# Kernel optimization log

Measured on AMD Instinct MI355X. Metric: run time of the kernel, lower is better.

## Reference

```python
import jax, jax.numpy as jnp
import numpy as np

WINDOW = 512      # sliding window size (causal: keys in [m-WINDOW+1, m])
NEG_INF = -1e30   # large negative instead of -inf for fp16/bf16 safety


def setup_inputs() -> dict:
    key = jax.random.key(0)
    kq, kk, kv = jax.random.split(key, 3)
    B, S, H, Hk, D = 1, 8192, 32, 8, 128
    q = jax.random.normal(kq, (B, S, H, D), dtype=jnp.float32)
    k = jax.random.normal(kk, (B, S, Hk, D), dtype=jnp.float32)
    v = jax.random.normal(kv, (B, S, Hk, D), dtype=jnp.float32)
    return {"q": q, "k": k, "v": v}


def _swa_causal(q, k, v, window):
    """Causal sliding-window attention with GQA, banded (no SxS matrix)."""
    B, S, H, D = q.shape
    Hk = k.shape[2]
    G = H // Hk                      # query heads per kv head
    C = window                        # query block size
    nb = S // C                       # number of query blocks (S divisible by C here)
    L = 2 * window - 1                # kv window width per query block
    pad = window - 1
    scale = 1.0 / jnp.sqrt(jnp.asarray(D, q.dtype))

    # pad keys/values at the front so every block can gather a full window
    kp = jnp.pad(k, ((0, 0), (pad, 0), (0, 0), (0, 0)))
    vp = jnp.pad(v, ((0, 0), (pad, 0), (0, 0), (0, 0)))

    # block queries: [B, nb, C, Hk, G, D]
    qb = q.reshape(B, nb, C, Hk, G, D)

    # kv windows: block n sees padded positions [n*C, n*C + L)
    starts = jnp.arange(nb) * C                      # [nb]
    idx = starts[:, None] + jnp.arange(L)[None, :]   # [nb, L] padded coords
    kw = kp[:, idx]                                  # [B, nb, L, Hk, D]
    vw = vp[:, idx]                                  # [B, nb, L, Hk, D]

    # banded scores: [B, nb, Hk, G, C, L]
    scores = jnp.einsum('bnchgd,bnlhd->bnhgcl', qb, kw) * scale

    # mask: query i (global m = n*C + i), kv slot j (global n_pos = n*C + j - pad)
    # causal window: i <= j <= i + window - 1 ; plus n_pos >= 0
    i = jnp.arange(C)
    j = jnp.arange(L)
    band = (j[None, :] >= i[:, None]) & (j[None, :] <= i[:, None] + window - 1)  # [C, L]
    valid_n = (starts[:, None] + j[None, :] - pad) >= 0                          # [nb, L]
    mask = band[None, :, :] & valid_n[:, None, :]                                # [nb, C, L]

    scores = jnp.where(mask[:, None, None, :, :][None], scores, NEG_INF)
    p = jax.nn.softmax(scores, axis=-1)              # [B, nb, Hk, G, C, L]

    o = jnp.einsum('bnhgcl,bnlhd->bnchgd', p, vw)    # [B, nb, C, Hk, G, D]
    return o.reshape(B, S, H, D)


def reference(q, k, v):
    return _swa_causal(q, k, v, WINDOW)
```

## Files before the change

kernel.cpp:

```cpp
#include <hip/hip_runtime.h>

#define NH   32
#define NHK  8
#define D    128
#define QB   64
#define KB   64
#define NT   128

typedef float f32x4 __attribute__((ext_vector_type(4)));
typedef short bf16x8 __attribute__((ext_vector_type(8)));
typedef unsigned int uint4v __attribute__((ext_vector_type(4)));

__device__ __forceinline__ unsigned cvtpk(float lo, float hi) {
  unsigned r;
  asm("v_cvt_pk_bf16_f32 %0, %1, %2" : "=v"(r) : "v"(lo), "v"(hi));
  return r;
}
__device__ __forceinline__ void gload16(const void* g, void* l) {
  __builtin_amdgcn_global_load_lds(
      (__attribute__((address_space(1))) void*)g,
      (__attribute__((address_space(3))) void*)l, 16, 0, 0);
}

__device__ __forceinline__ int kidx(int j, int col) {
  return (((j >> 1) << 8) + ((j & 1) << 7) + col) ^ (((j >> 1) & 15) << 3);
}
__device__ __forceinline__ int vidx(int d, int j) {
  return (((d >> 1) << 7) + ((d & 1) << 6) + j) ^ (((d >> 1) & 15) << 3);
}

__global__ __launch_bounds__(256)
void prep_kv(const float* __restrict__ kg, const float* __restrict__ vg,
             short* __restrict__ kpre, short* __restrict__ vpre)
{
  int blk = blockIdx.x;
  int tid = threadIdx.x;
  bool isV = blk >= (NHK * NT);
  int lb   = isV ? blk - NHK * NT : blk;
  int hk   = lb >> 7;
  int t    = lb & 127;
  if (!isV) {
    int j  = tid >> 2;
    int dq = (tid & 3) * 32;
    const float* kp = kg + ((size_t)(t*KB + j) * NHK + hk) * D + dq;
    short* dst = kpre + (((size_t)(hk*NT + t)) << 13);
    #pragma unroll
    for (int c = 0; c < 4; ++c) {
      float4 a  = *(const float4*)(kp + c*8);
      float4 b2 = *(const float4*)(kp + c*8 + 4);
      uint4v u;
      u[0] = cvtpk(a.x, a.y);   u[1] = cvtpk(a.z, a.w);
      u[2] = cvtpk(b2.x, b2.y); u[3] = cvtpk(b2.z, b2.w);
      *(uint4v*)&dst[kidx(j, dq + c*8)] = u;
    }
  } else {
    int d0 = (tid & 31) * 4;
    int j0 = (tid >> 5) * 8;
    float tv[8][4];
    #pragma unroll
    for (int r = 0; r < 8; ++r) {
      float4 x = *(const float4*)(vg + ((size_t)(t*KB + j0 + r) * NHK + hk) * D + d0);
      tv[r][0]=x.x; tv[r][1]=x.y; tv[r][2]=x.z; tv[r][3]=x.w;
    }
    short* dst = vpre + (((size_t)(hk*NT + t)) << 13);
    #pragma unroll
    for (int c = 0; c < 4; ++c) {
      int d = d0 + c;
      uint4v u;
      u[0] = cvtpk(tv[0][c], tv[1][c]);
      u[1] = cvtpk(tv[2][c], tv[3][c]);
      u[2] = cvtpk(tv[4][c], tv[5][c]);
      u[3] = cvtpk(tv[6][c], tv[7][c]);
      *(uint4v*)&dst[vidx(d, j0)] = u;
    }
  }
}

__global__ __launch_bounds__(256, 3)
void swa_fwd(const float* __restrict__ qg, const short* __restrict__ kpre,
             const short* __restrict__ vpre, float* __restrict__ og)
{
  __shared__ __align__(16) short lds_k[KB * D];
  __shared__ __align__(16) short lds_v[KB * D];

  const int tid  = threadIdx.x;
  const int lane = tid & 63;
  const int w    = tid >> 6;
  const int il16 = lane & 15;
  const int g    = lane >> 4;

  int b    = blockIdx.x;
  int lidx = (b & 7) * 512 + (b >> 3);
  int hk   = lidx >> 9;
  int rem  = lidx & 511;
  int bq   = rem >> 2;
  int h    = hk * 4 + (rem & 3);
  int qs   = bq * QB;

  const float qscale = 0.088388347648318447f * 1.4426950408889634f;

  bf16x8 qf[4];
  {
    const float* qp = qg + ((size_t)(qs + 16*w + il16) * NH + h) * D + 8*g;
    #pragma unroll
    for (int ks = 0; ks < 4; ++ks) {
      float4 a = *(const float4*)(qp + 32*ks);
      float4 c = *(const float4*)(qp + 32*ks + 4);
      uint4v u;
      u[0] = cvtpk(a.x*qscale, a.y*qscale);
      u[1] = cvtpk(a.z*qscale, a.w*qscale);
      u[2] = cvtpk(c.x*qscale, c.y*qscale);
      u[3] = cvtpk(c.z*qscale, c.w*qscale);
      qf[ks] = __builtin_bit_cast(bf16x8, u);
    }
  }

  f32x4 acc_o[8];
  #pragma unroll
  for (int dt = 0; dt < 8; ++dt)
    #pragma unroll
    for (int r = 0; r < 4; ++r) acc_o[dt][r] = 0.0f;

  float l0 = 0.0f, l1 = 0.0f, l2 = 0.0f, l3 = 0.0f;

  const int iw_min = qs + 16*w;
  int t_lo = qs >= 512 ? (qs - 512) >> 6 : 0;
  int t_hi = qs >> 6;

  const short* gkb = kpre + (((size_t)hk * NT) << 13);
  const short* gvb = vpre + (((size_t)hk * NT) << 13);
  const int lo = w * 2048;
  const int go = lo + lane * 8;

  for (int t = t_lo; t <= t_hi; ++t) {
    const int kt = t * KB;

    {
      const short* gk = gkb + ((size_t)t << 13);
      const short* gv = gvb + ((size_t)t << 13);
      #pragma unroll
      for (int i = 0; i < 4; ++i) gload16(gk + go + i*512, &lds_k[0] + lo + i*512);
      #pragma unroll
      for (int i = 0; i < 4; ++i) gload16(gv + go + i*512, &lds_v[0] + lo + i*512);
    }
    asm volatile("s_waitcnt vmcnt(0)" ::: "memory");
    __builtin_amdgcn_s_barrier();
    __builtin_amdgcn_sched_barrier(0);

    bool skip = (kt > iw_min + 15) || (kt + KB - 1 < iw_min - 511);
    if (!skip) {
      f32x4 acc_s[4];
      #pragma unroll
      for (int jt = 0; jt < 4; ++jt)
        #pragma unroll
        for (int r = 0; r < 4; ++r) acc_s[jt][r] = 0.0f;

      __builtin_amdgcn_s_setprio(1);
      #pragma unroll
      for (int ks = 0; ks < 4; ++ks) {
        #pragma unroll
        for (int jt = 0; jt < 4; ++jt) {
          bf16x8 a = *(const bf16x8*)&lds_k[kidx(16*jt + il16, 32*ks + 8*g)];
          acc_s[jt] = __builtin_amdgcn_mfma_f32_16x16x32_bf16(a, qf[ks], acc_s[jt], 0, 0, 0);
        }
      }
      __builtin_amdgcn_s_setprio(0);

      bool do_causal = (kt + KB - 1 > iw_min);
      bool do_window = (kt < iw_min + 15 - 511);
      if (do_causal || do_window) {
        int base0 = kt - iw_min + 4*g - il16;
        #pragma unroll
        for (int jt = 0; jt < 4; ++jt)
          #pragma unroll
          for (int r = 0; r < 4; ++r) {
            int delta = base0 + 16*jt + r;
            if ((do_causal && delta > 0) || (do_window && delta < -511))
              acc_s[jt][r] = -1e30f;
          }
      }

      float p[4][4];
      #pragma unroll
      for (int jt = 0; jt < 4; ++jt)
        #pragma unroll
        for (int r = 0; r < 4; ++r)
          p[jt][r] = __builtin_amdgcn_exp2f(acc_s[jt][r]);
      l0 += p[0][0] + p[1][0] + p[2][0] + p[3][0];
      l1 += p[0][1] + p[1][1] + p[2][1] + p[3][1];
      l2 += p[0][2] + p[1][2] + p[2][2] + p[3][2];
      l3 += p[0][3] + p[1][3] + p[2][3] + p[3][3];

      #pragma unroll
      for (int kstep = 0; kstep < 2; ++kstep) {
        unsigned A0 = cvtpk(p[2*kstep+0][0], p[2*kstep+0][1]);
        unsigned B0 = cvtpk(p[2*kstep+0][2], p[2*kstep+0][3]);
        unsigned C0 = cvtpk(p[2*kstep+1][0], p[2*kstep+1][1]);
        unsigned D0 = cvtpk(p[2*kstep+1][2], p[2*kstep+1][3]);
        asm("v_permlane32_swap_b32 %0, %1" : "+v"(A0), "+v"(C0));
        asm("v_permlane32_swap_b32 %0, %1" : "+v"(B0), "+v"(D0));
        asm("v_permlane16_swap_b32 %0, %1" : "+v"(A0), "+v"(C0));
        asm("v_permlane16_swap_b32 %0, %1" : "+v"(B0), "+v"(D0));
        uint4v pu; pu[0] = A0; pu[1] = B0; pu[2] = C0; pu[3] = D0;
        bf16x8 pb = __builtin_bit_cast(bf16x8, pu);

        __builtin_amdgcn_s_setprio(1);
        #pragma unroll
        for (int dt = 0; dt < 8; ++dt) {
          bf16x8 a = *(const bf16x8*)&lds_v[vidx(16*dt + il16, 32*kstep + 8*g)];
          acc_o[dt] = __builtin_amdgcn_mfma_f32_16x16x32_bf16(a, pb, acc_o[dt], 0, 0, 0);
        }
        __builtin_amdgcn_s_setprio(0);
      }
    }
    if (t < t_hi) __builtin_amdgcn_s_barrier();
  }

  float l_lane = (l0 + l1) + (l2 + l3);
  l_lane += __shfl_xor(l_lane, 16);
  l_lane += __shfl_xor(l_lane, 32);
  float inv_l = 1.0f / l_lane;

  const size_t orow = ((size_t)(qs + 16*w + il16) * NH + h) * D;
  #pragma unroll
  for (int dt = 0; dt < 8; ++dt) {
    float4 o;
    o.x = acc_o[dt][0] * inv_l;
    o.y = acc_o[dt][1] * inv_l;
    o.z = acc_o[dt][2] * inv_l;
    o.w = acc_o[dt][3] * inv_l;
    *(float4*)(og + orow + 16*dt + 4*g) = o;
  }
}

typedef float f32x16 __attribute__((ext_vector_type(16)));

__global__ __launch_bounds__(256, 2)
void swa_fwd_fb(const float* __restrict__ qg, const float* __restrict__ kg,
                const float* __restrict__ vg, float* __restrict__ og)
{
  __shared__ __align__(16) short lds_k[KB * D];
  __shared__ __align__(16) short lds_v[D * KB];

  const int tid  = threadIdx.x;
  const int lane = tid & 63;
  const int w    = tid >> 6;
  const int il   = lane & 31;
  const int half = lane >> 5;

  int b    = blockIdx.x;
  int lidx = (b & 7) * 256 + (b >> 3);
  int hk   = lidx >> 8;
  int rem  = lidx & 255;
  int bq   = rem >> 2;
  int h    = hk * 4 + (rem & 3);
  int qs   = bq * 128;

  const float qscale = 0.088388347648318447f * 1.4426950408889634f;

  bf16x8 qf[8];
  {
    const float* qp = qg + ((size_t)(qs + 32*w + il) * NH + h) * D + half * 8;
    #pragma unroll
    for (int ks = 0; ks < 8; ++ks) {
      float4 a = *(const float4*)(qp + ks*16);
      float4 c = *(const float4*)(qp + ks*16 + 4);
      uint4v u;
      u[0] = cvtpk(a.x*qscale, a.y*qscale);
      u[1] = cvtpk(a.z*qscale, a.w*qscale);
      u[2] = cvtpk(c.x*qscale, c.y*qscale);
      u[3] = cvtpk(c.z*qscale, c.w*qscale);
      qf[ks] = __builtin_bit_cast(bf16x8, u);
    }
  }

  f32x16 acc_o[4];
  #pragma unroll
  for (int dt = 0; dt < 4; ++dt)
    #pragma unroll
    for (int r = 0; r < 16; ++r) acc_o[dt][r] = 0.0f;

  float l0 = 0.0f, l1 = 0.0f, l2 = 0.0f, l3 = 0.0f;

  int t_lo = 2*bq - 8; if (t_lo < 0) t_lo = 0;
  int t_hi = 2*bq + 1;
  const int iw_min = qs + 32*w;

  for (int t = t_lo; t <= t_hi; ++t) {
    const int kt = t * KB;
    {
      int j  = tid >> 2;
      int dq = (tid & 3) * 32;
      const float* kp = kg + ((size_t)(kt + j) * NHK + hk) * D + dq;
      #pragma unroll
      for (int c = 0; c < 4; ++c) {
        float4 a  = *(const float4*)(kp + c*8);
        float4 d2 = *(const float4*)(kp + c*8 + 4);
        uint4v u;
        u[0] = cvtpk(a.x, a.y);   u[1] = cvtpk(a.z, a.w);
        u[2] = cvtpk(d2.x, d2.y); u[3] = cvtpk(d2.z, d2.w);
        *(uint4v*)&lds_k[kidx(j, dq + c*8)] = u;
      }
    }
    {
      int d0 = (tid & 31) * 4;
      int j0 = (tid >> 5) * 8;
      float tv[8][4];
      #pragma unroll
      for (int r = 0; r < 8; ++r) {
        float4 x = *(const float4*)(vg + ((size_t)(kt + j0 + r) * NHK + hk) * D + d0);
        tv[r][0]=x.x; tv[r][1]=x.y; tv[r][2]=x.z; tv[r][3]=x.w;
      }
      #pragma unroll
      for (int c = 0; c < 4; ++c) {
        int d = d0 + c;
        uint4v u;
        u[0] = cvtpk(tv[0][c], tv[1][c]);
        u[1] = cvtpk(tv[2][c], tv[3][c]);
        u[2] = cvtpk(tv[4][c], tv[5][c]);
        u[3] = cvtpk(tv[6][c], tv[7][c]);
        *(uint4v*)&lds_v[vidx(d, j0)] = u;
      }
    }
    __syncthreads();

    bool skip = (kt > iw_min + 31) || (kt + KB - 1 < iw_min - 511);
    if (!skip) {
      f32x16 acc_s[2];
      #pragma unroll
      for (int mt = 0; mt < 2; ++mt)
        #pragma unroll
        for (int r = 0; r < 16; ++r) acc_s[mt][r] = 0.0f;

      #pragma unroll
      for (int ks = 0; ks < 8; ++ks) {
        #pragma unroll
        for (int mt = 0; mt < 2; ++mt) {
          int jrow = mt*32 + il;
          bf16x8 a = *(const bf16x8*)&lds_k[kidx(jrow, ks*16 + half*8)];
          acc_s[mt] = __builtin_amdgcn_mfma_f32_32x32x16_bf16(a, qf[ks], acc_s[mt], 0, 0, 0);
        }
      }

      bool do_causal = (kt + KB - 1 > iw_min);
      bool do_window = (kt < iw_min + 31 - 511);
      if (do_causal || do_window) {
        int base0 = kt - iw_min - il + 4*half;
        #pragma unroll
        for (int mt = 0; mt < 2; ++mt)
          #pragma unroll
          for (int r = 0; r < 16; ++r) {
            int delta = base0 + 32*mt + (r & 3) + 8*(r >> 2);
            if ((do_causal && delta > 0) || (do_window && delta < -511))
              acc_s[mt][r] = -1e30f;
          }
      }

      #pragma unroll
      for (int mt = 0; mt < 2; ++mt) {
        float p[16];
        #pragma unroll
        for (int r = 0; r < 16; ++r)
          p[r] = __builtin_amdgcn_exp2f(acc_s[mt][r]);
        l0 += p[0] + p[4];  l1 += p[1] + p[5];
        l2 += p[2] + p[6];  l3 += p[3] + p[7];
        l0 += p[8] + p[12]; l1 += p[9] + p[13];
        l2 += p[10]+ p[14]; l3 += p[11]+ p[15];

        unsigned pkw[8];
        #pragma unroll
        for (int hb = 0; hb < 2; ++hb) {
          int bs = hb * 8;
          unsigned X1 = cvtpk(p[bs+0], p[bs+1]);
          unsigned X2 = cvtpk(p[bs+2], p[bs+3]);
          unsigned Y1 = cvtpk(p[bs+4], p[bs+5]);
          unsigned Y2 = cvtpk(p[bs+6], p[bs+7]);
          asm("v_permlane32_swap_b32 %0, %1" : "+v"(X1), "+v"(Y1));
          asm("v_permlane32_swap_b32 %0, %1" : "+v"(X2), "+v"(Y2));
          pkw[hb*4 + 0] = X1; pkw[hb*4 + 1] = X2;
          pkw[hb*4 + 2] = Y1; pkw[hb*4 + 3] = Y2;
        }
        #pragma unroll
        for (int ksl = 0; ksl < 2; ++ksl) {
          int ks = mt*2 + ksl;
          uint4v pu;
          pu[0] = pkw[ksl*4+0]; pu[1] = pkw[ksl*4+1];
          pu[2] = pkw[ksl*4+2]; pu[3] = pkw[ksl*4+3];
          bf16x8 pb = __builtin_bit_cast(bf16x8, pu);
          #pragma unroll
          for (int dt = 0; dt < 4; ++dt) {
            int d = dt*32 + il;
            bf16x8 a = *(const bf16x8*)&lds_v[vidx(d, ks*16 + half*8)];
            acc_o[dt] = __builtin_amdgcn_mfma_f32_32x32x16_bf16(a, pb, acc_o[dt], 0, 0, 0);
          }
        }
      }
    }
    __syncthreads();
  }

  float l_lane = (l0 + l1) + (l2 + l3);
  float l_tot  = l_lane + __shfl_xor(l_lane, 32);
  float inv_l  = 1.0f / l_tot;
  const size_t orow = ((size_t)(qs + 32*w + il) * NH + h) * D;
  #pragma unroll
  for (int dt = 0; dt < 4; ++dt)
    #pragma unroll
    for (int rg = 0; rg < 4; ++rg) {
      float4 o;
      o.x = acc_o[dt][rg*4+0] * inv_l;
      o.y = acc_o[dt][rg*4+1] * inv_l;
      o.z = acc_o[dt][rg*4+2] * inv_l;
      o.w = acc_o[dt][rg*4+3] * inv_l;
      *(float4*)(og + orow + dt*32 + 8*rg + 4*half) = o;
    }
}

extern "C" void kernel_launch(void* const* d_in, const int* in_sizes, int n_in,
                              void* d_out, int out_size, void* d_ws, size_t ws_size,
                              hipStream_t stream) {
  const float* q = (const float*)d_in[0];
  const float* k = (const float*)d_in[1];
  const float* v = (const float*)d_in[2];
  float* o = (float*)d_out;
  const size_t per = (size_t)NHK * NT * KB * D;
  const size_t need = 2 * per * sizeof(short);
  if (ws_size >= need) {
    short* kpre = (short*)d_ws;
    short* vpre = kpre + per;
    hipLaunchKernelGGL(prep_kv, dim3(2 * NHK * NT), dim3(256), 0, stream, k, v, kpre, vpre);
    hipLaunchKernelGGL(swa_fwd, dim3(4096), dim3(256), 0, stream, q, kpre, vpre, o);
  } else {
    hipLaunchKernelGGL(swa_fwd_fb, dim3(2048), dim3(256), 0, stream, q, k, v, o);
  }
}
```

Measured before the change: 143.5 us.

## Double-buffer K tiles and prefetch next K/V during compute

Doubles the K shared-memory buffer so the next K tile streams in while QK^T for the current tile runs. The next V tile is loaded right after the PV step, so it overlaps the next iteration's QK and softmax. Staged waitcnt and barrier pairs guard each buffer. The per-wave skip of fully masked tiles is removed, because every wave must now reach the barriers; this adds some wasted MFMA work on edge tiles.

```diff
diff --git a/kernel.cpp b/kernel.cpp
--- a/kernel.cpp
+++ b/kernel.cpp
@@ -80,7 +80,7 @@
 void swa_fwd(const float* __restrict__ qg, const short* __restrict__ kpre,
              const short* __restrict__ vpre, float* __restrict__ og)
 {
-  __shared__ __align__(16) short lds_k[KB * D];
+  __shared__ __align__(16) short lds_k[2][KB * D];
   __shared__ __align__(16) short lds_v[KB * D];
 
   const int tid  = threadIdx.x;
@@ -132,88 +132,113 @@
   const int lo = w * 2048;
   const int go = lo + lane * 8;
 
+  asm volatile("s_waitcnt vmcnt(0)" ::: "memory");
+  {
+    const short* gk = gkb + ((size_t)t_lo << 13);
+    const short* gv = gvb + ((size_t)t_lo << 13);
+    short* lk = &lds_k[t_lo & 1][0];
+    #pragma unroll
+    for (int i = 0; i < 4; ++i) gload16(gk + go + i*512, lk + lo + i*512);
+    #pragma unroll
+    for (int i = 0; i < 4; ++i) gload16(gv + go + i*512, &lds_v[0] + lo + i*512);
+  }
+  asm volatile("s_waitcnt vmcnt(0)" ::: "memory");
+  __builtin_amdgcn_s_barrier();
+  __builtin_amdgcn_sched_barrier(0);
+
   for (int t = t_lo; t <= t_hi; ++t) {
-    const int kt = t * KB;
-
-    {
-      const short* gk = gkb + ((size_t)t << 13);
-      const short* gv = gvb + ((size_t)t << 13);
-      #pragma unroll
-      for (int i = 0; i < 4; ++i) gload16(gk + go + i*512, &lds_k[0] + lo + i*512);
-      #pragma unroll
-      for (int i = 0; i < 4; ++i) gload16(gv + go + i*512, &lds_v[0] + lo + i*512);
-    }
-    asm volatile("s_waitcnt vmcnt(0)" ::: "memory");
-    __builtin_amdgcn_s_barrier();
-    __builtin_amdgcn_sched_barrier(0);
-
-    bool skip = (kt > iw_min + 15) || (kt + KB - 1 < iw_min - 511);
-    if (!skip) {
-      f32x4 acc_s[4];
+    const int kt  = t * KB;
+    const int cur = t & 1;
+
+    if (t < t_hi) {
+      const short* gk = gkb + ((size_t)(t+1) << 13);
+      short* lk = &lds_k[cur ^ 1][0];
+      #pragma unroll
+      for (int i = 0; i < 4; ++i) gload16(gk + go + i*512, lk + lo + i*512);
+    }
+
+    f32x4 acc_s[4];
+    #pragma unroll
+    for (int jt = 0; jt < 4; ++jt)
+      #pragma unroll
+      for (int r = 0; r < 4; ++r) acc_s[jt][r] = 0.0f;
+
+    __builtin_amdgcn_s_setprio(1);
+    #pragma unroll
+    for (int ks = 0; ks < 4; ++ks) {
+      #pragma unroll
+      for (int jt = 0; jt < 4; ++jt) {
+        bf16x8 a = *(const bf16x8*)&lds_k[cur][kidx(16*jt + il16, 32*ks + 8*g)];
+        acc_s[jt] = __builtin_amdgcn_mfma_f32_16x16x32_bf16(a, qf[ks], acc_s[jt], 0, 0, 0);
+      }
+    }
+    __builtin_amdgcn_s_setprio(0);
+
+    bool do_causal = (kt + KB - 1 > iw_min);
+    bool do_window = (kt < iw_min + 15 - 511);
+    if (do_causal || do_window) {
+      int base0 = kt - iw_min + 4*g - il16;
       #pragma unroll
       for (int jt = 0; jt < 4; ++jt)
         #pragma unroll
-        for (int r = 0; r < 4; ++r) acc_s[jt][r] = 0.0f;
+        for (int r = 0; r < 4; ++r) {
+          int delta = base0 + 16*jt + r;
+          if ((do_causal && delta > 0) || (do_window && delta < -511))
+            acc_s[jt][r] = -1e30f;
+        }
+    }
+
+    float p[4][4];
+    #pragma unroll
+    for (int jt = 0; jt < 4; ++jt)
+      #pragma unroll
+      for (int r = 0; r < 4; ++r)
+        p[jt][r] = __builtin_amdgcn_exp2f(acc_s[jt][r]);
+    l0 += p[0][0] + p[1][0] + p[2][0] + p[3][0];
+    l1 += p[0][1] + p[1][1] + p[2][1] + p[3][1];
+    l2 += p[0][2] + p[1][2] + p[2][2] + p[3][2];
+    l3 += p[0][3] + p[1][3] + p[2][3] + p[3][3];
+
+    if (t > t_lo) {
+      if (t < t_hi) asm volatile("s_waitcnt vmcnt(4)" ::: "memory");
+      else          asm volatile("s_waitcnt vmcnt(0)" ::: "memory");
+      __builtin_amdgcn_s_barrier();
+      __builtin_amdgcn_sched_barrier(0);
+    }
+
+    #pragma unroll
+    for (int kstep = 0; kstep < 2; ++kstep) {
+      unsigned A0 = cvtpk(p[2*kstep+0][0], p[2*kstep+0][1]);
+      unsigned B0 = cvtpk(p[2*kstep+0][2], p[2*kstep+0][3]);
+      unsigned C0 = cvtpk(p[2*kstep+1][0], p[2*kstep+1][1]);
+      unsigned D0 = cvtpk(p[2*kstep+1][2], p[2*kstep+1][3]);
+      asm("v_permlane32_swap_b32 %0, %1" : "+v"(A0), "+v"(C0));
+      asm("v_permlane32_swap_b32 %0, %1" : "+v"(B0), "+v"(D0));
+      asm("v_permlane16_swap_b32 %0, %1" : "+v"(A0), "+v"(C0));
+      asm("v_permlane16_swap_b32 %0, %1" : "+v"(B0), "+v"(D0));
+      uint4v pu; pu[0] = A0; pu[1] = B0; pu[2] = C0; pu[3] = D0;
+      bf16x8 pb = __builtin_bit_cast(bf16x8, pu);
 
       __builtin_amdgcn_s_setprio(1);
       #pragma unroll
-      for (int ks = 0; ks < 4; ++ks) {
-        #pragma unroll
-        for (int jt = 0; jt < 4; ++jt) {
-          bf16x8 a = *(const bf16x8*)&lds_k[kidx(16*jt + il16, 32*ks + 8*g)];
-          acc_s[jt] = __builtin_amdgcn_mfma_f32_16x16x32_bf16(a, qf[ks], acc_s[jt], 0, 0, 0);
-        }
+      for (int dt = 0; dt < 8; ++dt) {
+        bf16x8 a = *(const bf16x8*)&lds_v[vidx(16*dt + il16, 32*kstep + 8*g)];
+        acc_o[dt] = __builtin_amdgcn_mfma_f32_16x16x32_bf16(a, pb, acc_o[dt], 0, 0, 0);
       }
       __builtin_amdgcn_s_setprio(0);
-
-      bool do_causal = (kt + KB - 1 > iw_min);
-      bool do_window = (kt < iw_min + 15 - 511);
-      if (do_causal || do_window) {
-        int base0 = kt - iw_min + 4*g - il16;
-        #pragma unroll
-        for (int jt = 0; jt < 4; ++jt)
-          #pragma unroll
-          for (int r = 0; r < 4; ++r) {
-            int delta = base0 + 16*jt + r;
-            if ((do_causal && delta > 0) || (do_window && delta < -511))
-              acc_s[jt][r] = -1e30f;
-          }
-      }
-
-      float p[4][4];
-      #pragma unroll
-      for (int jt = 0; jt < 4; ++jt)
-        #pragma unroll
-        for (int r = 0; r < 4; ++r)
-          p[jt][r] = __builtin_amdgcn_exp2f(acc_s[jt][r]);
-      l0 += p[0][0] + p[1][0] + p[2][0] + p[3][0];
-      l1 += p[0][1] + p[1][1] + p[2][1] + p[3][1];
-      l2 += p[0][2] + p[1][2] + p[2][2] + p[3][2];
-      l3 += p[0][3] + p[1][3] + p[2][3] + p[3][3];
-
-      #pragma unroll
-      for (int kstep = 0; kstep < 2; ++kstep) {
-        unsigned A0 = cvtpk(p[2*kstep+0][0], p[2*kstep+0][1]);
-        unsigned B0 = cvtpk(p[2*kstep+0][2], p[2*kstep+0][3]);
-        unsigned C0 = cvtpk(p[2*kstep+1][0], p[2*kstep+1][1]);
-        unsigned D0 = cvtpk(p[2*kstep+1][2], p[2*kstep+1][3]);
-        asm("v_permlane32_swap_b32 %0, %1" : "+v"(A0), "+v"(C0));
-        asm("v_permlane32_swap_b32 %0, %1" : "+v"(B0), "+v"(D0));
-        asm("v_permlane16_swap_b32 %0, %1" : "+v"(A0), "+v"(C0));
-        asm("v_permlane16_swap_b32 %0, %1" : "+v"(B0), "+v"(D0));
-        uint4v pu; pu[0] = A0; pu[1] = B0; pu[2] = C0; pu[3] = D0;
-        bf16x8 pb = __builtin_bit_cast(bf16x8, pu);
-
-        __builtin_amdgcn_s_setprio(1);
-        #pragma unroll
-        for (int dt = 0; dt < 8; ++dt) {
-          bf16x8 a = *(const bf16x8*)&lds_v[vidx(16*dt + il16, 32*kstep + 8*g)];
-          acc_o[dt] = __builtin_amdgcn_mfma_f32_16x16x32_bf16(a, pb, acc_o[dt], 0, 0, 0);
-        }
-        __builtin_amdgcn_s_setprio(0);
-      }
-    }
-    if (t < t_hi) __builtin_amdgcn_s_barrier();
+    }
+
+    if (t < t_hi) {
+      __builtin_amdgcn_s_barrier();
+      {
+        const short* gv = gvb + ((size_t)(t+1) << 13);
+        #pragma unroll
+        for (int i = 0; i < 4; ++i) gload16(gv + go + i*512, &lds_v[0] + lo + i*512);
+      }
+      asm volatile("s_waitcnt vmcnt(4)" ::: "memory");
+      __builtin_amdgcn_s_barrier();
+      __builtin_amdgcn_sched_barrier(0);
+    }
   }
 
   float l_lane = (l0 + l1) + (l2 + l3);
```

New measurement: 144.6 us. No clear change (+0.8%).
